# Kernel optimization log

Measured on AMD Instinct MI355X. Metric: run time of the kernel, lower is better.

Reference implementation:

```python
import jax, jax.numpy as jnp
import numpy as np
from jax import lax

B, T, H, C = 1024, 1024, 256, 10

def setup_inputs() -> dict:
    key = jax.random.key(0)
    k = jax.random.split(key, 6)
    return {
        "x": jax.random.normal(k[0], (B, T), dtype=jnp.float32),
        "W_hx": jax.random.normal(k[1], (H, 1), dtype=jnp.float32),
        "W_hh": jax.random.normal(k[2], (H, H), dtype=jnp.float32),
        "b_h": jax.random.normal(k[3], (H,), dtype=jnp.float32),
        "W_hp": jax.random.normal(k[4], (C, H), dtype=jnp.float32),
        "b_o": jax.random.normal(k[5], (C,), dtype=jnp.float32),
    }

def reference(x, W_hx, W_hh, b_h, W_hp, b_o):
    # x: [B, T] (input_dim hard-coded to 1 in the original: x[:, t].unsqueeze(1))
    # torch.einsum('bh,hh->bh', h, W_hh) == h * diag(W_hh)  (repeated 'hh' index)
    w_diag = jnp.einsum('hh->h', W_hh)          # [H] loop-invariant, hoisted
    w_in = W_hx[:, 0]                            # [H]
    h0 = jnp.zeros((x.shape[0], w_in.shape[0]), dtype=x.dtype)

    def step(h, x_t):
        # einsum('bn,hn->bh', x_t[:,None], W_hx) with n=1 is an outer product
        h_new = jnp.tanh(x_t[:, None] * w_in + h * w_diag + b_h)
        return h_new, None

    h_final, _ = lax.scan(step, h0, x.T)         # scan over time: xs [T, B]
    return jnp.einsum('bh,ch->bc', h_final, W_hp) + b_o  # [B, C]
```

## Files before the change

### kernel.cpp

```cpp
#include <hip/hip_runtime.h>
#include <math.h>

#define BB 1024
#define TT 1024
#define HH 256
#define CC 10


typedef float f2 __attribute__((ext_vector_type(2)));

__global__ __launch_bounds__(HH) void vanilla_rnn_kernel(
    const float* __restrict__ x,
    const float* __restrict__ W_hx,
    const float* __restrict__ W_hh,
    const float* __restrict__ b_h,
    const float* __restrict__ W_hp,
    const float* __restrict__ b_o,
    float* __restrict__ out)
{
    __shared__ float part[2][CC * 4];

    const int tid = threadIdx.x;
    const int b0  = blockIdx.x * 2;

    const float S    = 2.88539008177792681472f;
    const float winS = W_hx[tid] * S;
    const float wd   = W_hh[tid * HH + tid];
    const float A    = -2.0f * wd * S;
    const float bhS2 = (b_h[tid] + wd) * S;
    float whp[CC];
#pragma unroll
    for (int c = 0; c < CC; ++c) whp[c] = W_hp[c * HH + tid];

    const float4* __restrict__ xA = (const float4*)(x + (size_t)b0 * TT);
    const float4* __restrict__ xB = (const float4*)(x + (size_t)(b0 + 1) * TT);

    f2 r  = (f2){0.5f, 0.5f};
    const f2 A2   = (f2){A, A};
    const f2 one2 = (f2){1.0f, 1.0f};

    float4 curA = xA[0], curB = xB[0];
    float4 nxtA = xA[1], nxtB = xB[1];

#pragma unroll 2
    for (int i = 0; i < TT / 4; ++i) {
        int ip = i + 2;
        if (ip > TT / 4 - 1) ip = TT / 4 - 1;
        float4 pfA = xA[ip];
        float4 pfB = xB[ip];

        f2 q, m, t, u;
#define STEP(XA, XB)                                   \
        q.x = fmaf((XA), winS, bhS2);                  \
        q.y = fmaf((XB), winS, bhS2);                  \
        m   = __builtin_elementwise_fma(A2, r, q);     \
        t.x = __builtin_amdgcn_exp2f(m.x);             \
        t.y = __builtin_amdgcn_exp2f(m.y);             \
        u   = t + one2;                                \
        r.x = __builtin_amdgcn_rcpf(u.x);              \
        r.y = __builtin_amdgcn_rcpf(u.y);

        STEP(curA.x, curB.x)
        STEP(curA.y, curB.y)
        STEP(curA.z, curB.z)
        STEP(curA.w, curB.w)
#undef STEP

        curA = nxtA; curB = nxtB;
        nxtA = pfA;  nxtB = pfB;
    }
    float h0 = fmaf(-2.0f, r.x, 1.0f);
    float h1 = fmaf(-2.0f, r.y, 1.0f);

    const int lane = tid & 63;
    const int wave = tid >> 6;
#pragma unroll
    for (int c = 0; c < CC; ++c) {
        float v0 = h0 * whp[c];
        float v1 = h1 * whp[c];
#pragma unroll
        for (int off = 32; off >= 1; off >>= 1) {
            v0 += __shfl_down(v0, off);
            v1 += __shfl_down(v1, off);
        }
        if (lane == 0) { part[0][c * 4 + wave] = v0; part[1][c * 4 + wave] = v1; }
    }
    __syncthreads();

    if (tid < 2 * CC) {
        const int bb = tid / CC;
        const int c  = tid - bb * CC;
        float acc = b_o[c];
#pragma unroll
        for (int w = 0; w < 4; ++w) acc += part[bb][c * 4 + w];
        out[(size_t)(b0 + bb) * CC + c] = acc;
    }
}

extern "C" void kernel_launch(void* const* d_in, const int* in_sizes, int n_in,
                              void* d_out, int out_size, void* d_ws, size_t ws_size,
                              hipStream_t stream) {
    const float* x    = (const float*)d_in[0];
    const float* W_hx = (const float*)d_in[1];
    const float* W_hh = (const float*)d_in[2];
    const float* b_h  = (const float*)d_in[3];
    const float* W_hp = (const float*)d_in[4];
    const float* b_o  = (const float*)d_in[5];
    float* out = (float*)d_out;

    vanilla_rnn_kernel<<<BB / 2, HH, 0, stream>>>(x, W_hx, W_hh, b_h, W_hp, b_o, out);
}
```

Baseline: 129.0 us.

## Stage input rows in LDS and replace rcp with Newton-iteration reciprocal

```diff
diff --git a/kernel.cpp b/kernel.cpp
--- a/kernel.cpp
+++ b/kernel.cpp
@@ -18,10 +18,19 @@
     const float* __restrict__ b_o,
     float* __restrict__ out)
 {
+    __shared__ float xs0[TT + 8];
+    __shared__ float xs1[TT + 8];
     __shared__ float part[2][CC * 4];
 
     const int tid = threadIdx.x;
     const int b0  = blockIdx.x * 2;
+
+    ((float4*)xs0)[tid] = ((const float4*)(x + (size_t)b0 * TT))[tid];
+    ((float4*)xs1)[tid] = ((const float4*)(x + (size_t)(b0 + 1) * TT))[tid];
+    if (tid < 2) {
+        ((float4*)xs0)[TT / 4 + tid] = make_float4(0.f, 0.f, 0.f, 0.f);
+        ((float4*)xs1)[TT / 4 + tid] = make_float4(0.f, 0.f, 0.f, 0.f);
+    }
 
     const float S    = 2.88539008177792681472f;
     const float winS = W_hx[tid] * S;
@@ -32,33 +41,35 @@
 #pragma unroll
     for (int c = 0; c < CC; ++c) whp[c] = W_hp[c * HH + tid];
 
-    const float4* __restrict__ xA = (const float4*)(x + (size_t)b0 * TT);
-    const float4* __restrict__ xB = (const float4*)(x + (size_t)(b0 + 1) * TT);
+    __syncthreads();
 
-    f2 r  = (f2){0.5f, 0.5f};
+    f2 r = (f2){0.5f, 0.5f};
     const f2 A2   = (f2){A, A};
     const f2 one2 = (f2){1.0f, 1.0f};
+    const f2 two2 = (f2){2.0f, 2.0f};
 
-    float4 curA = xA[0], curB = xB[0];
-    float4 nxtA = xA[1], nxtB = xB[1];
+    const float4* xa = (const float4*)xs0;
+    const float4* xb = (const float4*)xs1;
+    float4 curA = xa[0], nxtA = xa[1];
+    float4 curB = xb[0], nxtB = xb[1];
+#pragma unroll 4
+    for (int t4 = 0; t4 < TT / 4; ++t4) {
+        float4 pfA = xa[t4 + 2];
+        float4 pfB = xb[t4 + 2];
 
-#pragma unroll 2
-    for (int i = 0; i < TT / 4; ++i) {
-        int ip = i + 2;
-        if (ip > TT / 4 - 1) ip = TT / 4 - 1;
-        float4 pfA = xA[ip];
-        float4 pfB = xB[ip];
-
-        f2 q, m, t, u;
-#define STEP(XA, XB)                                   \
-        q.x = fmaf((XA), winS, bhS2);                  \
-        q.y = fmaf((XB), winS, bhS2);                  \
-        m   = __builtin_elementwise_fma(A2, r, q);     \
-        t.x = __builtin_amdgcn_exp2f(m.x);             \
-        t.y = __builtin_amdgcn_exp2f(m.y);             \
-        u   = t + one2;                                \
-        r.x = __builtin_amdgcn_rcpf(u.x);              \
-        r.y = __builtin_amdgcn_rcpf(u.y);
+        f2 q, m, t, u, y, e;
+#define STEP(XA, XB)                                            \
+        q.x = fmaf((XA), winS, bhS2);                           \
+        q.y = fmaf((XB), winS, bhS2);                           \
+        m   = __builtin_elementwise_fma(A2, r, q);              \
+        t.x = __builtin_amdgcn_exp2f(m.x);                      \
+        t.y = __builtin_amdgcn_exp2f(m.y);                      \
+        u   = t + one2;                                         \
+        y.x = __uint_as_float(0x7EF311C3u - __float_as_uint(u.x)); \
+        y.y = __uint_as_float(0x7EF311C3u - __float_as_uint(u.y)); \
+        e   = __builtin_elementwise_fma(-u, y, two2); y = y * e;   \
+        e   = __builtin_elementwise_fma(-u, y, two2); y = y * e;   \
+        e   = __builtin_elementwise_fma(-u, y, two2); r = y * e;
 
         STEP(curA.x, curB.x)
         STEP(curA.y, curB.y)
```

Result: slower. 133.3 us (+3.3%).

## Process four batch rows per block and stage inputs in shared memory

Applied to the files above, without the earlier changes.

```diff
diff --git a/kernel.cpp b/kernel.cpp
--- a/kernel.cpp
+++ b/kernel.cpp
@@ -5,11 +5,10 @@
 #define TT 1024
 #define HH 256
 #define CC 10
+#define RB 4
 
 
-typedef float f2 __attribute__((ext_vector_type(2)));
-
-__global__ __launch_bounds__(HH) void vanilla_rnn_kernel(
+__global__ __launch_bounds__(HH, 1) void vanilla_rnn_kernel(
     const float* __restrict__ x,
     const float* __restrict__ W_hx,
     const float* __restrict__ W_hh,
@@ -18,10 +17,17 @@
     const float* __restrict__ b_o,
     float* __restrict__ out)
 {
-    __shared__ float part[2][CC * 4];
+    __shared__ float xs[RB][TT + 8];
+    __shared__ float part[RB][CC * 4];
 
     const int tid = threadIdx.x;
-    const int b0  = blockIdx.x * 2;
+    const int b0  = blockIdx.x * RB;
+
+#pragma unroll
+    for (int rr = 0; rr < RB; ++rr) {
+        ((float4*)xs[rr])[tid] = ((const float4*)(x + (size_t)(b0 + rr) * TT))[tid];
+        if (tid < 2) ((float4*)xs[rr])[TT / 4 + tid] = make_float4(0.f, 0.f, 0.f, 0.f);
+    }
 
     const float S    = 2.88539008177792681472f;
     const float winS = W_hx[tid] * S;
@@ -32,45 +38,52 @@
 #pragma unroll
     for (int c = 0; c < CC; ++c) whp[c] = W_hp[c * HH + tid];
 
-    const float4* __restrict__ xA = (const float4*)(x + (size_t)b0 * TT);
-    const float4* __restrict__ xB = (const float4*)(x + (size_t)(b0 + 1) * TT);
+    __syncthreads();
 
-    f2 r  = (f2){0.5f, 0.5f};
-    const f2 A2   = (f2){A, A};
-    const f2 one2 = (f2){1.0f, 1.0f};
+    const float4* x0 = (const float4*)xs[0];
+    const float4* x1 = (const float4*)xs[1];
+    const float4* x2 = (const float4*)xs[2];
+    const float4* x3 = (const float4*)xs[3];
 
-    float4 curA = xA[0], curB = xB[0];
-    float4 nxtA = xA[1], nxtB = xB[1];
+    float r0 = 0.5f, r1 = 0.5f, r2 = 0.5f, r3 = 0.5f;
 
-#pragma unroll 2
-    for (int i = 0; i < TT / 4; ++i) {
-        int ip = i + 2;
-        if (ip > TT / 4 - 1) ip = TT / 4 - 1;
-        float4 pfA = xA[ip];
-        float4 pfB = xB[ip];
+#define STEP4(E0, E1, E2, E3) {                         \
+        float q0 = fmaf((E0), winS, bhS2);              \
+        float q1 = fmaf((E1), winS, bhS2);              \
+        float q2 = fmaf((E2), winS, bhS2);              \
+        float q3 = fmaf((E3), winS, bhS2);              \
+        float m0 = fmaf(A, r0, q0);                     \
+        float m1 = fmaf(A, r1, q1);                     \
+        float m2 = fmaf(A, r2, q2);                     \
+        float m3 = fmaf(A, r3, q3);                     \
+        float t0 = __builtin_amdgcn_exp2f(m0);          \
+        float t1 = __builtin_amdgcn_exp2f(m1);          \
+        float t2 = __builtin_amdgcn_exp2f(m2);          \
+        float t3 = __builtin_amdgcn_exp2f(m3);          \
+        r0 = __builtin_amdgcn_rcpf(t0 + 1.0f);          \
+        r1 = __builtin_amdgcn_rcpf(t1 + 1.0f);          \
+        r2 = __builtin_amdgcn_rcpf(t2 + 1.0f);          \
+        r3 = __builtin_amdgcn_rcpf(t3 + 1.0f); }
 
-        f2 q, m, t, u;
-#define STEP(XA, XB)                                   \
-        q.x = fmaf((XA), winS, bhS2);                  \
-        q.y = fmaf((XB), winS, bhS2);                  \
-        m   = __builtin_elementwise_fma(A2, r, q);     \
-        t.x = __builtin_amdgcn_exp2f(m.x);             \
-        t.y = __builtin_amdgcn_exp2f(m.y);             \
-        u   = t + one2;                                \
-        r.x = __builtin_amdgcn_rcpf(u.x);              \
-        r.y = __builtin_amdgcn_rcpf(u.y);
+    float4 va0 = x0[0], va1 = x1[0], va2 = x2[0], va3 = x3[0];
+    for (int i = 0; i < TT / 4; i += 2) {
+        float4 vb0 = x0[i + 1], vb1 = x1[i + 1], vb2 = x2[i + 1], vb3 = x3[i + 1];
+        STEP4(va0.x, va1.x, va2.x, va3.x)
+        STEP4(va0.y, va1.y, va2.y, va3.y)
+        STEP4(va0.z, va1.z, va2.z, va3.z)
+        STEP4(va0.w, va1.w, va2.w, va3.w)
+        va0 = x0[i + 2]; va1 = x1[i + 2]; va2 = x2[i + 2]; va3 = x3[i + 2];
+        STEP4(vb0.x, vb1.x, vb2.x, vb3.x)
+        STEP4(vb0.y, vb1.y, vb2.y, vb3.y)
+        STEP4(vb0.z, vb1.z, vb2.z, vb3.z)
+        STEP4(vb0.w, vb1.w, vb2.w, vb3.w)
+    }
+#undef STEP4
 
-        STEP(curA.x, curB.x)
-        STEP(curA.y, curB.y)
-        STEP(curA.z, curB.z)
-        STEP(curA.w, curB.w)
-#undef STEP
-
-        curA = nxtA; curB = nxtB;
-        nxtA = pfA;  nxtB = pfB;
-    }
-    float h0 = fmaf(-2.0f, r.x, 1.0f);
-    float h1 = fmaf(-2.0f, r.y, 1.0f);
+    const float h0 = fmaf(-2.0f, r0, 1.0f);
+    const float h1 = fmaf(-2.0f, r1, 1.0f);
+    const float h2 = fmaf(-2.0f, r2, 1.0f);
+    const float h3 = fmaf(-2.0f, r3, 1.0f);
 
     const int lane = tid & 63;
     const int wave = tid >> 6;
@@ -78,16 +91,25 @@
     for (int c = 0; c < CC; ++c) {
         float v0 = h0 * whp[c];
         float v1 = h1 * whp[c];
+        float v2 = h2 * whp[c];
+        float v3 = h3 * whp[c];
 #pragma unroll
         for (int off = 32; off >= 1; off >>= 1) {
             v0 += __shfl_down(v0, off);
             v1 += __shfl_down(v1, off);
+            v2 += __shfl_down(v2, off);
+            v3 += __shfl_down(v3, off);
         }
-        if (lane == 0) { part[0][c * 4 + wave] = v0; part[1][c * 4 + wave] = v1; }
+        if (lane == 0) {
+            part[0][c * 4 + wave] = v0;
+            part[1][c * 4 + wave] = v1;
+            part[2][c * 4 + wave] = v2;
+            part[3][c * 4 + wave] = v3;
+        }
     }
     __syncthreads();
 
-    if (tid < 2 * CC) {
+    if (tid < RB * CC) {
         const int bb = tid / CC;
         const int c  = tid - bb * CC;
         float acc = b_o[c];
@@ -108,5 +130,5 @@
     const float* b_o  = (const float*)d_in[5];
     float* out = (float*)d_out;
 
-    vanilla_rnn_kernel<<<BB / 2, HH, 0, stream>>>(x, W_hx, W_hh, b_h, W_hp, b_o, out);
+    vanilla_rnn_kernel<<<BB / RB, HH, 0, stream>>>(x, W_hx, W_hh, b_h, W_hp, b_o, out);
 }
```

After: 125.1 us. 3.0% less time.

## Stage interleaved x pairs in LDS and use packed FMA for input term

Applied to the files above, without the earlier changes.

```diff
diff --git a/kernel.cpp b/kernel.cpp
--- a/kernel.cpp
+++ b/kernel.cpp
@@ -8,6 +8,7 @@
 
 
 typedef float f2 __attribute__((ext_vector_type(2)));
+typedef float f4 __attribute__((ext_vector_type(4)));
 
 __global__ __launch_bounds__(HH) void vanilla_rnn_kernel(
     const float* __restrict__ x,
@@ -18,59 +19,58 @@
     const float* __restrict__ b_o,
     float* __restrict__ out)
 {
+    __shared__ f4 xsp[TT / 2 + 2];
     __shared__ float part[2][CC * 4];
 
     const int tid = threadIdx.x;
     const int b0  = blockIdx.x * 2;
 
+    {
+        f4 a4 = ((const f4*)(x + (size_t)b0 * TT))[tid];
+        f4 b4 = ((const f4*)(x + (size_t)(b0 + 1) * TT))[tid];
+        xsp[2 * tid]     = (f4){a4.x, b4.x, a4.y, b4.y};
+        xsp[2 * tid + 1] = (f4){a4.z, b4.z, a4.w, b4.w};
+        if (tid < 2) xsp[TT / 2 + tid] = (f4){0.f, 0.f, 0.f, 0.f};
+    }
+
     const float S    = 2.88539008177792681472f;
     const float winS = W_hx[tid] * S;
     const float wd   = W_hh[tid * HH + tid];
-    const float A    = -2.0f * wd * S;
     const float bhS2 = (b_h[tid] + wd) * S;
+    const f2 A2   = (f2){-2.0f * wd * S, -2.0f * wd * S};
+    const f2 win2 = (f2){winS, winS};
+    const f2 bh2  = (f2){bhS2, bhS2};
+    const f2 one2 = (f2){1.0f, 1.0f};
     float whp[CC];
 #pragma unroll
     for (int c = 0; c < CC; ++c) whp[c] = W_hp[c * HH + tid];
 
-    const float4* __restrict__ xA = (const float4*)(x + (size_t)b0 * TT);
-    const float4* __restrict__ xB = (const float4*)(x + (size_t)(b0 + 1) * TT);
+    __syncthreads();
 
-    f2 r  = (f2){0.5f, 0.5f};
-    const f2 A2   = (f2){A, A};
-    const f2 one2 = (f2){1.0f, 1.0f};
+    f2 r = (f2){0.5f, 0.5f};
 
-    float4 curA = xA[0], curB = xB[0];
-    float4 nxtA = xA[1], nxtB = xB[1];
+#define STEP(XPAIR) {                                   \
+        f2 xv = (XPAIR);                                \
+        f2 q  = __builtin_elementwise_fma(xv, win2, bh2); \
+        f2 m  = __builtin_elementwise_fma(A2, r, q);    \
+        f2 t;                                           \
+        t.x = __builtin_amdgcn_exp2f(m.x);              \
+        t.y = __builtin_amdgcn_exp2f(m.y);              \
+        f2 u = t + one2;                                \
+        r.x = __builtin_amdgcn_rcpf(u.x);               \
+        r.y = __builtin_amdgcn_rcpf(u.y); }
 
-#pragma unroll 2
-    for (int i = 0; i < TT / 4; ++i) {
-        int ip = i + 2;
-        if (ip > TT / 4 - 1) ip = TT / 4 - 1;
-        float4 pfA = xA[ip];
-        float4 pfB = xB[ip];
-
-        f2 q, m, t, u;
-#define STEP(XA, XB)                                   \
-        q.x = fmaf((XA), winS, bhS2);                  \
-        q.y = fmaf((XB), winS, bhS2);                  \
-        m   = __builtin_elementwise_fma(A2, r, q);     \
-        t.x = __builtin_amdgcn_exp2f(m.x);             \
-        t.y = __builtin_amdgcn_exp2f(m.y);             \
-        u   = t + one2;                                \
-        r.x = __builtin_amdgcn_rcpf(u.x);              \
-        r.y = __builtin_amdgcn_rcpf(u.y);
-
-        STEP(curA.x, curB.x)
-        STEP(curA.y, curB.y)
-        STEP(curA.z, curB.z)
-        STEP(curA.w, curB.w)
+    f4 va = xsp[0], vb = xsp[1];
+    for (int k = 0; k < TT / 2; k += 4) {
+        f4 vc = xsp[k + 2], vd = xsp[k + 3];
+        STEP(va.xy) STEP(va.zw) STEP(vb.xy) STEP(vb.zw)
+        va = xsp[k + 4]; vb = xsp[k + 5];
+        STEP(vc.xy) STEP(vc.zw) STEP(vd.xy) STEP(vd.zw)
+    }
 #undef STEP
 
-        curA = nxtA; curB = nxtB;
-        nxtA = pfA;  nxtB = pfB;
-    }
-    float h0 = fmaf(-2.0f, r.x, 1.0f);
-    float h1 = fmaf(-2.0f, r.y, 1.0f);
+    const float h0 = fmaf(-2.0f, r.x, 1.0f);
+    const float h1 = fmaf(-2.0f, r.y, 1.0f);
 
     const int lane = tid & 63;
     const int wave = tid >> 6;
```

Measured after the change: 110.5 us, median of 3. 14.4% less time.
